# Kernel tuning notes

Hardware: AMD Instinct MI355X
Metric: run time of the kernel (lower is better)

The kernel has to match this reference:

```python
import jax, jax.numpy as jnp
import numpy as np


def setup_inputs() -> dict:
    key = jax.random.key(0)
    ks = jax.random.split(key, 7)
    d_in, d_out, batch = 4096, 4096, 8192
    x = jax.random.normal(ks[0], (batch, d_in), dtype=jnp.float32)
    w_loc = jax.random.normal(ks[1], (d_in, d_out), dtype=jnp.float32) * (1.0 / np.sqrt(d_in))
    w_std = jnp.full((d_in, d_out), -6.0, dtype=jnp.float32) + 0.1 * jax.random.normal(ks[2], (d_in, d_out), dtype=jnp.float32)
    b_loc = jax.random.normal(ks[3], (1, d_out), dtype=jnp.float32) * 0.02
    b_std = jnp.full((1, d_out), -6.0, dtype=jnp.float32) + 0.1 * jax.random.normal(ks[4], (1, d_out), dtype=jnp.float32)
    eps_w = jax.random.normal(ks[5], (d_in, d_out), dtype=jnp.float32)
    eps_b = jax.random.normal(ks[6], (1, d_out), dtype=jnp.float32)
    return {"x": x, "w_loc": w_loc, "w_std": w_std, "b_loc": b_loc, "b_std": b_std, "eps_w": eps_w, "eps_b": eps_b}


def reference(x, w_loc, w_std, b_loc, b_std, eps_w, eps_b):
    # Reparameterized sample: W ~ Normal(w_loc, softplus(w_std))
    w = w_loc + jax.nn.softplus(w_std) * eps_w          # [d_in, d_out]
    b = b_loc + jax.nn.softplus(b_std) * eps_b          # [1, d_out]
    return x @ w + b                                    # [batch, d_out]
```

## Files before the change

kernel.cpp:

```cpp
#include <hip/hip_runtime.h>

typedef unsigned short u16;
typedef unsigned int u32;
typedef __bf16 bf16;
typedef __attribute__((ext_vector_type(8))) bf16 bf16x8;
typedef __attribute__((ext_vector_type(4))) float f32x4;
typedef __attribute__((ext_vector_type(8))) u16 u16x8;

#define M_DIM 8192
#define N_DIM 4096
#define K_DIM 4096
#define NT    (K_DIM / 32)

__device__ __forceinline__ u16 f2bf(float f) {
    u32 u = __float_as_uint(f);
    u32 r = (u + 0x7fffu + ((u >> 16) & 1u)) >> 16;
    return (u16)r;
}

__device__ __forceinline__ float softplus_f(float x) {
    return fmaxf(x, 0.f) + log1pf(expf(-fabsf(x)));
}

__device__ __forceinline__ void gload_lds16(const void* g, void* l) {
    __builtin_amdgcn_global_load_lds(
        (const __attribute__((address_space(1))) void*)g,
        (__attribute__((address_space(3))) void*)l,
        16, 0, 0);
}

__global__ void conv_x_kernel(const float* __restrict__ x, u16* __restrict__ xb,
                              long long n8) {
    long long idx = blockIdx.x * (long long)blockDim.x + threadIdx.x;
    long long stride = gridDim.x * (long long)blockDim.x;
    for (long long i = idx; i < n8; i += stride) {
        const float4* xp = (const float4*)(x + i * 8);
        float4 a = xp[0], b = xp[1];
        u16x8 r;
        r[0] = f2bf(a.x); r[1] = f2bf(a.y); r[2] = f2bf(a.z); r[3] = f2bf(a.w);
        r[4] = f2bf(b.x); r[5] = f2bf(b.y); r[6] = f2bf(b.z); r[7] = f2bf(b.w);
        *(u16x8*)(xb + i * 8) = r;
    }
}

__global__ void wconv_kernel(const float* __restrict__ w_loc,
                             const float* __restrict__ w_std,
                             const float* __restrict__ eps_w,
                             u16* __restrict__ wt) {
    __shared__ u16 t[64][66];
    const int kb = blockIdx.x & 63;
    const int nb = blockIdx.x >> 6;
    const int k0 = kb * 64, n0 = nb * 64;
    const int tx = threadIdx.x & 63;
    const int ty = threadIdx.x >> 6;
#pragma unroll
    for (int r = 0; r < 64; r += 4) {
        const size_t off = (size_t)(k0 + r + ty) * N_DIM + n0 + tx;
        float v = w_loc[off] + softplus_f(w_std[off]) * eps_w[off];
        t[r + ty][tx] = f2bf(v);
    }
    __syncthreads();
#pragma unroll
    for (int r = 0; r < 64; r += 4) {
        wt[(size_t)(n0 + r + ty) * K_DIM + k0 + tx] = t[tx][r + ty];
    }
}

__global__ void bias_kernel(const float* __restrict__ b_loc,
                            const float* __restrict__ b_std,
                            const float* __restrict__ eps_b,
                            float* __restrict__ bias) {
    int i = blockIdx.x * blockDim.x + threadIdx.x;
    if (i < N_DIM) bias[i] = b_loc[i] + softplus_f(b_std[i]) * eps_b[i];
}

__global__ __launch_bounds__(512, 2) void gemm_kernel(
    const u16* __restrict__ Xb, const u16* __restrict__ Wt,
    const float* __restrict__ bias, float* __restrict__ C) {
    __shared__ __align__(16) u16 lds[32768];

    const int tid = threadIdx.x;
    const int l  = tid & 63;
    const int w  = tid >> 6;
    const int wm = w >> 2;
    const int wn = w & 3;

    const int swz = (blockIdx.x & 7) * 64 + (blockIdx.x >> 3);
    const int m0 = (swz >> 4) * 256;
    const int n0 = (swz & 15) * 256;

    const u16* Ab = Xb + (size_t)m0 * K_DIM;
    const u16* Bb = Wt + (size_t)n0 * K_DIM;

    const int sr = w * 16 + (l >> 2);
    const int sc = ((l & 3) ^ ((l >> 3) & 3)) << 3;

    const int fr = l & 15, hi = l >> 4;
    const int ce = ((hi ^ ((fr >> 1) & 3)) << 3);

    auto stageA = [&](int buf, int half, int kt) {
        const u16* g = Ab + (size_t)(half * 128 + sr) * K_DIM + kt * 32 + sc;
        gload_lds16(g, &lds[buf * 8192 + half * 4096 + w * 512]);
    };
    auto stageB = [&](int buf, int half, int kt) {
        const u16* g = Bb + (size_t)(half * 128 + sr) * K_DIM + kt * 32 + sc;
        gload_lds16(g, &lds[16384 + buf * 8192 + half * 4096 + w * 512]);
    };
    auto ldA = [&](int buf, int m) -> bf16x8 {
        return *(const bf16x8*)&lds[buf * 8192 + wm * 4096 + (m * 16 + fr) * 32 + ce];
    };
    auto ldB = [&](int buf, int n) -> bf16x8 {
        return *(const bf16x8*)&lds[16384 + buf * 8192 + (wn >> 1) * 4096
                                    + ((wn & 1) * 64 + n * 16 + fr) * 32 + ce];
    };

    f32x4 acc[8][4] = {};

    stageA(0, 0, 0); stageA(0, 1, 0); stageB(0, 0, 0); stageB(0, 1, 0);
    stageB(1, 0, 1); stageB(1, 1, 1);
    asm volatile("s_waitcnt vmcnt(2)" ::: "memory");
    __builtin_amdgcn_sched_barrier(0);
    __builtin_amdgcn_s_barrier();

    for (int t = 0; t < NT; ++t) {
        const int buf = t & 1;

        bf16x8 b[4], a[4];
        b[0] = ldB(buf, 0); b[1] = ldB(buf, 1); b[2] = ldB(buf, 2); b[3] = ldB(buf, 3);
        a[0] = ldA(buf, 0); a[1] = ldA(buf, 1); a[2] = ldA(buf, 2); a[3] = ldA(buf, 3);
        if (t + 1 < NT) { stageA(buf ^ 1, 0, t + 1); stageA(buf ^ 1, 1, t + 1); }
        __builtin_amdgcn_s_barrier();
        asm volatile("s_waitcnt lgkmcnt(0)" ::: "memory");
        __builtin_amdgcn_sched_barrier(0);
        __builtin_amdgcn_s_setprio(1);
#pragma unroll
        for (int i = 0; i < 4; ++i)
#pragma unroll
            for (int n = 0; n < 4; ++n)
                acc[i][n] = __builtin_amdgcn_mfma_f32_16x16x32_bf16(
                    a[i], b[n], acc[i][n], 0, 0, 0);
        __builtin_amdgcn_s_setprio(0);
        __builtin_amdgcn_s_barrier();

        a[0] = ldA(buf, 4); a[1] = ldA(buf, 5); a[2] = ldA(buf, 6); a[3] = ldA(buf, 7);
        if (t + 2 < NT) { stageB(buf, 0, t + 2); stageB(buf, 1, t + 2); }
        __builtin_amdgcn_s_barrier();
        asm volatile("s_waitcnt lgkmcnt(0)" ::: "memory");
        __builtin_amdgcn_sched_barrier(0);
        __builtin_amdgcn_s_setprio(1);
#pragma unroll
        for (int i = 0; i < 4; ++i)
#pragma unroll
            for (int n = 0; n < 4; ++n)
                acc[4 + i][n] = __builtin_amdgcn_mfma_f32_16x16x32_bf16(
                    a[i], b[n], acc[4 + i][n], 0, 0, 0);
        __builtin_amdgcn_s_setprio(0);
        if (t + 2 < NT) {
            asm volatile("s_waitcnt vmcnt(2)" ::: "memory");
        } else if (t + 1 < NT) {
            asm volatile("s_waitcnt vmcnt(0)" ::: "memory");
        }
        __builtin_amdgcn_sched_barrier(0);
        __builtin_amdgcn_s_barrier();
    }

    const int orow0 = m0 + wm * 128;
    const int ocol0 = n0 + wn * 64;
    float bv[4];
#pragma unroll
    for (int n = 0; n < 4; ++n) bv[n] = bias[ocol0 + n * 16 + fr];
#pragma unroll
    for (int m = 0; m < 8; ++m)
#pragma unroll
        for (int n = 0; n < 4; ++n)
#pragma unroll
            for (int j = 0; j < 4; ++j)
                C[(size_t)(orow0 + m * 16 + hi * 4 + j) * N_DIM
                  + ocol0 + n * 16 + fr] = acc[m][n][j] + bv[n];
}

extern "C" void kernel_launch(void* const* d_in, const int* in_sizes, int n_in,
                              void* d_out, int out_size, void* d_ws, size_t ws_size,
                              hipStream_t stream) {
    const float* x     = (const float*)d_in[0];
    const float* w_loc = (const float*)d_in[1];
    const float* w_std = (const float*)d_in[2];
    const float* b_loc = (const float*)d_in[3];
    const float* b_std = (const float*)d_in[4];
    const float* eps_w = (const float*)d_in[5];
    const float* eps_b = (const float*)d_in[6];
    float* out = (float*)d_out;

    char* ws = (char*)d_ws;
    u16* Xb   = (u16*)ws;
    u16* Wt   = (u16*)(ws + (size_t)M_DIM * K_DIM * 2);
    float* bv = (float*)(ws + (size_t)M_DIM * K_DIM * 2
                            + (size_t)N_DIM * K_DIM * 2);

    conv_x_kernel<<<2048, 256, 0, stream>>>(x, Xb, (long long)M_DIM * K_DIM / 8);
    wconv_kernel<<<(K_DIM / 64) * (N_DIM / 64), 256, 0, stream>>>(w_loc, w_std, eps_w, Wt);
    bias_kernel<<<N_DIM / 256, 256, 0, stream>>>(b_loc, b_std, eps_b, bv);
    gemm_kernel<<<(M_DIM / 256) * (N_DIM / 256), 512, 0, stream>>>(Xb, Wt, bv, out);
}
```

Before: 354.9 us.

## Deepen GEMM K-tile to 64 with 8-way XOR-swizzled LDS layout

Doubles the K depth of each staged tile from 32 to 64 and moves LDS to 128KB of dynamic shared memory. The LDS layout changes to 64-element rows with an 8-way XOR swizzle, and each iteration now runs four MFMA phases split across the two K halves. The aim is fewer loop iterations and vmcnt waits per K, plus longer contiguous global loads. The trade-off is that 128KB of LDS per block likely allows only one block per CU instead of the two requested by launch bounds, which reduces latency hiding.

```diff
diff --git a/kernel.cpp b/kernel.cpp
--- a/kernel.cpp
+++ b/kernel.cpp
@@ -10,7 +10,7 @@
 #define M_DIM 8192
 #define N_DIM 4096
 #define K_DIM 4096
-#define NT    (K_DIM / 32)
+#define NTK   (K_DIM / 64)
 
 __device__ __forceinline__ u16 f2bf(float f) {
     u32 u = __float_as_uint(f);
@@ -74,10 +74,26 @@
     if (i < N_DIM) bias[i] = b_loc[i] + softplus_f(b_std[i]) * eps_b[i];
 }
 
+#define MFMA_Q(O, AV, BV)                                                    \
+    _Pragma("unroll") for (int i_ = 0; i_ < 4; ++i_)                         \
+    _Pragma("unroll") for (int n_ = 0; n_ < 4; ++n_)                         \
+        acc[(O) + i_][n_] = __builtin_amdgcn_mfma_f32_16x16x32_bf16(         \
+            AV[i_], BV[n_], acc[(O) + i_][n_], 0, 0, 0);
+
+#define PH_SYNC_IN()                                                         \
+    __builtin_amdgcn_s_barrier();                                            \
+    asm volatile("s_waitcnt lgkmcnt(0)" ::: "memory");                       \
+    __builtin_amdgcn_sched_barrier(0);                                       \
+    __builtin_amdgcn_s_setprio(1);
+
+#define PH_SYNC_OUT()                                                        \
+    __builtin_amdgcn_s_setprio(0);                                           \
+    __builtin_amdgcn_s_barrier();
+
 __global__ __launch_bounds__(512, 2) void gemm_kernel(
     const u16* __restrict__ Xb, const u16* __restrict__ Wt,
     const float* __restrict__ bias, float* __restrict__ C) {
-    __shared__ __align__(16) u16 lds[32768];
+    extern __shared__ u16 lds[];
 
     const int tid = threadIdx.x;
     const int l  = tid & 63;
@@ -92,72 +108,82 @@
     const u16* Ab = Xb + (size_t)m0 * K_DIM;
     const u16* Bb = Wt + (size_t)n0 * K_DIM;
 
-    const int sr = w * 16 + (l >> 2);
-    const int sc = ((l & 3) ^ ((l >> 3) & 3)) << 3;
+    const int srow = tid >> 3;
+    const int sq   = ((tid & 7) ^ (srow & 7)) * 8;
 
     const int fr = l & 15, hi = l >> 4;
-    const int ce = ((hi ^ ((fr >> 1) & 3)) << 3);
-
-    auto stageA = [&](int buf, int half, int kt) {
-        const u16* g = Ab + (size_t)(half * 128 + sr) * K_DIM + kt * 32 + sc;
-        gload_lds16(g, &lds[buf * 8192 + half * 4096 + w * 512]);
+    const int cg0 = (hi ^ (fr & 7)) * 8;
+    const int cg1 = cg0 ^ 32;
+
+    auto stageA = [&](int u) {
+#pragma unroll
+        for (int s = 0; s < 4; ++s) {
+            const u16* g = Ab + (size_t)(s * 64 + srow) * K_DIM + u * 64 + sq;
+            gload_lds16(g, &lds[(u & 1) * 16384 + s * 4096 + tid * 8]);
+        }
     };
-    auto stageB = [&](int buf, int half, int kt) {
-        const u16* g = Bb + (size_t)(half * 128 + sr) * K_DIM + kt * 32 + sc;
-        gload_lds16(g, &lds[16384 + buf * 8192 + half * 4096 + w * 512]);
+    auto stageB = [&](int u) {
+#pragma unroll
+        for (int s = 0; s < 4; ++s) {
+            const u16* g = Bb + (size_t)(s * 64 + srow) * K_DIM + u * 64 + sq;
+            gload_lds16(g, &lds[32768 + (u & 1) * 16384 + s * 4096 + tid * 8]);
+        }
     };
-    auto ldA = [&](int buf, int m) -> bf16x8 {
-        return *(const bf16x8*)&lds[buf * 8192 + wm * 4096 + (m * 16 + fr) * 32 + ce];
-    };
-    auto ldB = [&](int buf, int n) -> bf16x8 {
-        return *(const bf16x8*)&lds[16384 + buf * 8192 + (wn >> 1) * 4096
-                                    + ((wn & 1) * 64 + n * 16 + fr) * 32 + ce];
-    };
 
     f32x4 acc[8][4] = {};
 
-    stageA(0, 0, 0); stageA(0, 1, 0); stageB(0, 0, 0); stageB(0, 1, 0);
-    stageB(1, 0, 1); stageB(1, 1, 1);
-    asm volatile("s_waitcnt vmcnt(2)" ::: "memory");
+    stageA(0); stageB(0); stageB(1);
+    asm volatile("s_waitcnt vmcnt(4)" ::: "memory");
     __builtin_amdgcn_sched_barrier(0);
     __builtin_amdgcn_s_barrier();
 
-    for (int t = 0; t < NT; ++t) {
-        const int buf = t & 1;
-
-        bf16x8 b[4], a[4];
-        b[0] = ldB(buf, 0); b[1] = ldB(buf, 1); b[2] = ldB(buf, 2); b[3] = ldB(buf, 3);
-        a[0] = ldA(buf, 0); a[1] = ldA(buf, 1); a[2] = ldA(buf, 2); a[3] = ldA(buf, 3);
-        if (t + 1 < NT) { stageA(buf ^ 1, 0, t + 1); stageA(buf ^ 1, 1, t + 1); }
+    for (int u = 0; u < NTK; ++u) {
+        const int bo = (u & 1) * 16384;
+        const int bB = 32768 + bo;
+        const int arow = bo + (wm * 128 + fr) * 64;
+        const int brow = bB + (wn * 64 + fr) * 64;
+        bf16x8 a[4], b0[4], b1[4];
+
+#pragma unroll
+        for (int n = 0; n < 4; ++n) {
+            b0[n] = *(const bf16x8*)&lds[brow + n * 1024 + cg0];
+            b1[n] = *(const bf16x8*)&lds[brow + n * 1024 + cg1];
+        }
+#pragma unroll
+        for (int m = 0; m < 4; ++m)
+            a[m] = *(const bf16x8*)&lds[arow + m * 1024 + cg0];
+        if (u + 1 < NTK) stageA(u + 1);
+        PH_SYNC_IN();
+        MFMA_Q(0, a, b0);
+        PH_SYNC_OUT();
+
+#pragma unroll
+        for (int m = 0; m < 4; ++m)
+            a[m] = *(const bf16x8*)&lds[arow + (m + 4) * 1024 + cg0];
+        if (u + 2 < NTK) stageB(u + 2);
+        PH_SYNC_IN();
+        MFMA_Q(4, a, b0);
+        PH_SYNC_OUT();
+
+#pragma unroll
+        for (int m = 0; m < 4; ++m)
+            a[m] = *(const bf16x8*)&lds[arow + m * 1024 + cg1];
+        PH_SYNC_IN();
+        MFMA_Q(0, a, b1);
+        PH_SYNC_OUT();
+
+#pragma unroll
+        for (int m = 0; m < 4; ++m)
+            a[m] = *(const bf16x8*)&lds[arow + (m + 4) * 1024 + cg1];
         __builtin_amdgcn_s_barrier();
         asm volatile("s_waitcnt lgkmcnt(0)" ::: "memory");
         __builtin_amdgcn_sched_barrier(0);
         __builtin_amdgcn_s_setprio(1);
-#pragma unroll
-        for (int i = 0; i < 4; ++i)
-#pragma unroll
-            for (int n = 0; n < 4; ++n)
-                acc[i][n] = __builtin_amdgcn_mfma_f32_16x16x32_bf16(
-                    a[i], b[n], acc[i][n], 0, 0, 0);
+        MFMA_Q(4, a, b1);
         __builtin_amdgcn_s_setprio(0);
-        __builtin_amdgcn_s_barrier();
-
-        a[0] = ldA(buf, 4); a[1] = ldA(buf, 5); a[2] = ldA(buf, 6); a[3] = ldA(buf, 7);
-        if (t + 2 < NT) { stageB(buf, 0, t + 2); stageB(buf, 1, t + 2); }
-        __builtin_amdgcn_s_barrier();
-        asm volatile("s_waitcnt lgkmcnt(0)" ::: "memory");
-        __builtin_amdgcn_sched_barrier(0);
-        __builtin_amdgcn_s_setprio(1);
-#pragma unroll
-        for (int i = 0; i < 4; ++i)
-#pragma unroll
-            for (int n = 0; n < 4; ++n)
-                acc[4 + i][n] = __builtin_amdgcn_mfma_f32_16x16x32_bf16(
-                    a[i], b[n], acc[4 + i][n], 0, 0, 0);
-        __builtin_amdgcn_s_setprio(0);
-        if (t + 2 < NT) {
-            asm volatile("s_waitcnt vmcnt(2)" ::: "memory");
-        } else if (t + 1 < NT) {
+        if (u + 2 < NTK) {
+            asm volatile("s_waitcnt vmcnt(4)" ::: "memory");
+        } else if (u + 1 < NTK) {
             asm volatile("s_waitcnt vmcnt(0)" ::: "memory");
         }
         __builtin_amdgcn_sched_barrier(0);
@@ -197,8 +223,11 @@
     float* bv = (float*)(ws + (size_t)M_DIM * K_DIM * 2
                             + (size_t)N_DIM * K_DIM * 2);
 
+    (void)hipFuncSetAttribute((const void*)gemm_kernel,
+                              hipFuncAttributeMaxDynamicSharedMemorySize, 131072);
+
     conv_x_kernel<<<2048, 256, 0, stream>>>(x, Xb, (long long)M_DIM * K_DIM / 8);
     wconv_kernel<<<(K_DIM / 64) * (N_DIM / 64), 256, 0, stream>>>(w_loc, w_std, eps_w, Wt);
     bias_kernel<<<N_DIM / 256, 256, 0, stream>>>(b_loc, b_std, eps_b, bv);
-    gemm_kernel<<<(M_DIM / 256) * (N_DIM / 256), 512, 0, stream>>>(Xb, Wt, bv, out);
-}
+    gemm_kernel<<<(M_DIM / 256) * (N_DIM / 256), 512, 131072, stream>>>(Xb, Wt, bv, out);
+}
```

After: 354.6 us. About the same (-0.1%).

## Deepen GEMM K-tile to 64 with triple-buffered B in dynamic LDS

Applied to the files above, without the earlier changes.

The GEMM main loop now processes 64-wide K tiles with a 128-byte-row XOR swizzle. A is double-buffered and B is triple-buffered in 160KB of dynamic shared memory. Each half-step issues 32 MFMAs per wave with a single barrier per iteration, cutting synchronisation and LDS-load overhead per unit of K. The larger LDS footprint likely limits residency to one block per CU, reducing latency hiding from co-resident blocks.

```diff
diff --git a/kernel.cpp b/kernel.cpp
--- a/kernel.cpp
+++ b/kernel.cpp
@@ -10,7 +10,7 @@
 #define M_DIM 8192
 #define N_DIM 4096
 #define K_DIM 4096
-#define NT    (K_DIM / 32)
+#define NTK   (K_DIM / 64)
 
 __device__ __forceinline__ u16 f2bf(float f) {
     u32 u = __float_as_uint(f);
@@ -77,7 +77,7 @@
 __global__ __launch_bounds__(512, 2) void gemm_kernel(
     const u16* __restrict__ Xb, const u16* __restrict__ Wt,
     const float* __restrict__ bias, float* __restrict__ C) {
-    __shared__ __align__(16) u16 lds[32768];
+    extern __shared__ __align__(16) u16 lds[];
 
     const int tid = threadIdx.x;
     const int l  = tid & 63;
@@ -92,91 +92,100 @@
     const u16* Ab = Xb + (size_t)m0 * K_DIM;
     const u16* Bb = Wt + (size_t)n0 * K_DIM;
 
-    const int sr = w * 16 + (l >> 2);
-    const int sc = ((l & 3) ^ ((l >> 3) & 3)) << 3;
+    const int srow = tid >> 3;
+    const int sq   = ((tid & 7) ^ (srow & 7)) * 8;
 
     const int fr = l & 15, hi = l >> 4;
-    const int ce = ((hi ^ ((fr >> 1) & 3)) << 3);
-
-    auto stageA = [&](int buf, int half, int kt) {
-        const u16* g = Ab + (size_t)(half * 128 + sr) * K_DIM + kt * 32 + sc;
-        gload_lds16(g, &lds[buf * 8192 + half * 4096 + w * 512]);
+    const int g0 = (hi ^ (fr & 7)) << 3;
+
+    auto stageA = [&](int u, int h) {
+#pragma unroll
+        for (int s = 0; s < 2; ++s) {
+            const u16* g = Ab + (size_t)(h * 128 + s * 64 + srow) * K_DIM + u * 64 + sq;
+            gload_lds16(g, &lds[(u & 1) * 16384 + h * 8192 + s * 4096 + tid * 8]);
+        }
     };
-    auto stageB = [&](int buf, int half, int kt) {
-        const u16* g = Bb + (size_t)(half * 128 + sr) * K_DIM + kt * 32 + sc;
-        gload_lds16(g, &lds[16384 + buf * 8192 + half * 4096 + w * 512]);
+    auto stageB = [&](int u, int slot, int h) {
+#pragma unroll
+        for (int s = 0; s < 2; ++s) {
+            const u16* g = Bb + (size_t)(h * 128 + s * 64 + srow) * K_DIM + u * 64 + sq;
+            gload_lds16(g, &lds[32768 + slot * 16384 + h * 8192 + s * 4096 + tid * 8]);
+        }
     };
-    auto ldA = [&](int buf, int m) -> bf16x8 {
-        return *(const bf16x8*)&lds[buf * 8192 + wm * 4096 + (m * 16 + fr) * 32 + ce];
-    };
-    auto ldB = [&](int buf, int n) -> bf16x8 {
-        return *(const bf16x8*)&lds[16384 + buf * 8192 + (wn >> 1) * 4096
-                                    + ((wn & 1) * 64 + n * 16 + fr) * 32 + ce];
-    };
 
     f32x4 acc[8][4] = {};
 
-    stageA(0, 0, 0); stageA(0, 1, 0); stageB(0, 0, 0); stageB(0, 1, 0);
-    stageB(1, 0, 1); stageB(1, 1, 1);
-    asm volatile("s_waitcnt vmcnt(2)" ::: "memory");
+    stageA(0, 0); stageA(0, 1);
+    stageB(0, 0, 0); stageB(0, 0, 1);
+    stageB(1, 1, 0); stageB(1, 1, 1);
+    asm volatile("s_waitcnt vmcnt(4)" ::: "memory");
     __builtin_amdgcn_sched_barrier(0);
     __builtin_amdgcn_s_barrier();
 
-    for (int t = 0; t < NT; ++t) {
-        const int buf = t & 1;
-
-        bf16x8 b[4], a[4];
-        b[0] = ldB(buf, 0); b[1] = ldB(buf, 1); b[2] = ldB(buf, 2); b[3] = ldB(buf, 3);
-        a[0] = ldA(buf, 0); a[1] = ldA(buf, 1); a[2] = ldA(buf, 2); a[3] = ldA(buf, 3);
-        if (t + 1 < NT) { stageA(buf ^ 1, 0, t + 1); stageA(buf ^ 1, 1, t + 1); }
-        __builtin_amdgcn_s_barrier();
+#define MFMA32()                                                              \
+    _Pragma("unroll") for (int mb = 0; mb < 8; ++mb)                          \
+    _Pragma("unroll") for (int nb = 0; nb < 4; ++nb)                          \
+        acc[mb][nb] = __builtin_amdgcn_mfma_f32_16x16x32_bf16(                \
+            a[mb], b[nb], acc[mb][nb], 0, 0, 0);
+
+    int scur = 0, snxt = 2;
+    for (int u = 0; u < NTK; ++u) {
+        const int ab = (u & 1) * 16384 + (wm * 128 + fr) * 64;
+        const int bb = 32768 + scur * 16384 + (wn * 64 + fr) * 64;
+        bf16x8 a[8], b[4];
+
+#pragma unroll
+        for (int nb = 0; nb < 4; ++nb)
+            b[nb] = *(const bf16x8*)&lds[bb + nb * 1024 + g0];
+#pragma unroll
+        for (int mb = 0; mb < 8; ++mb)
+            a[mb] = *(const bf16x8*)&lds[ab + mb * 1024 + g0];
+        if (u + 1 < NTK) { stageA(u + 1, 0); stageA(u + 1, 1); }
         asm volatile("s_waitcnt lgkmcnt(0)" ::: "memory");
         __builtin_amdgcn_sched_barrier(0);
         __builtin_amdgcn_s_setprio(1);
-#pragma unroll
-        for (int i = 0; i < 4; ++i)
-#pragma unroll
-            for (int n = 0; n < 4; ++n)
-                acc[i][n] = __builtin_amdgcn_mfma_f32_16x16x32_bf16(
-                    a[i], b[n], acc[i][n], 0, 0, 0);
+        MFMA32();
         __builtin_amdgcn_s_setprio(0);
-        __builtin_amdgcn_s_barrier();
-
-        a[0] = ldA(buf, 4); a[1] = ldA(buf, 5); a[2] = ldA(buf, 6); a[3] = ldA(buf, 7);
-        if (t + 2 < NT) { stageB(buf, 0, t + 2); stageB(buf, 1, t + 2); }
-        __builtin_amdgcn_s_barrier();
+
+#pragma unroll
+        for (int nb = 0; nb < 4; ++nb)
+            b[nb] = *(const bf16x8*)&lds[bb + nb * 1024 + (g0 ^ 32)];
+#pragma unroll
+        for (int mb = 0; mb < 8; ++mb)
+            a[mb] = *(const bf16x8*)&lds[ab + mb * 1024 + (g0 ^ 32)];
+        if (u + 2 < NTK) { stageB(u + 2, snxt, 0); stageB(u + 2, snxt, 1); }
         asm volatile("s_waitcnt lgkmcnt(0)" ::: "memory");
         __builtin_amdgcn_sched_barrier(0);
         __builtin_amdgcn_s_setprio(1);
-#pragma unroll
-        for (int i = 0; i < 4; ++i)
-#pragma unroll
-            for (int n = 0; n < 4; ++n)
-                acc[4 + i][n] = __builtin_amdgcn_mfma_f32_16x16x32_bf16(
-                    a[i], b[n], acc[4 + i][n], 0, 0, 0);
+        MFMA32();
         __builtin_amdgcn_s_setprio(0);
-        if (t + 2 < NT) {
-            asm volatile("s_waitcnt vmcnt(2)" ::: "memory");
-        } else if (t + 1 < NT) {
+
+        if (u + 2 < NTK) {
+            asm volatile("s_waitcnt vmcnt(4)" ::: "memory");
+        } else if (u + 1 < NTK) {
             asm volatile("s_waitcnt vmcnt(0)" ::: "memory");
         }
         __builtin_amdgcn_sched_barrier(0);
         __builtin_amdgcn_s_barrier();
-    }
+
+        scur = (scur == 2) ? 0 : scur + 1;
+        snxt = (snxt == 2) ? 0 : snxt + 1;
+    }
+#undef MFMA32
 
     const int orow0 = m0 + wm * 128;
     const int ocol0 = n0 + wn * 64;
     float bv[4];
 #pragma unroll
-    for (int n = 0; n < 4; ++n) bv[n] = bias[ocol0 + n * 16 + fr];
-#pragma unroll
-    for (int m = 0; m < 8; ++m)
-#pragma unroll
-        for (int n = 0; n < 4; ++n)
+    for (int nb = 0; nb < 4; ++nb) bv[nb] = bias[ocol0 + nb * 16 + fr];
+#pragma unroll
+    for (int mb = 0; mb < 8; ++mb)
+#pragma unroll
+        for (int nb = 0; nb < 4; ++nb)
 #pragma unroll
             for (int j = 0; j < 4; ++j)
-                C[(size_t)(orow0 + m * 16 + hi * 4 + j) * N_DIM
-                  + ocol0 + n * 16 + fr] = acc[m][n][j] + bv[n];
+                C[(size_t)(orow0 + mb * 16 + hi * 4 + j) * N_DIM
+                  + ocol0 + nb * 16 + fr] = acc[mb][nb][j] + bv[nb];
 }
 
 extern "C" void kernel_launch(void* const* d_in, const int* in_sizes, int n_in,
@@ -197,8 +206,11 @@
     float* bv = (float*)(ws + (size_t)M_DIM * K_DIM * 2
                             + (size_t)N_DIM * K_DIM * 2);
 
+    (void)hipFuncSetAttribute((const void*)gemm_kernel,
+                              hipFuncAttributeMaxDynamicSharedMemorySize, 163840);
+
     conv_x_kernel<<<2048, 256, 0, stream>>>(x, Xb, (long long)M_DIM * K_DIM / 8);
     wconv_kernel<<<(K_DIM / 64) * (N_DIM / 64), 256, 0, stream>>>(w_loc, w_std, eps_w, Wt);
     bias_kernel<<<N_DIM / 256, 256, 0, stream>>>(b_loc, b_std, eps_b, bv);
-    gemm_kernel<<<(M_DIM / 256) * (N_DIM / 256), 512, 0, stream>>>(Xb, Wt, bv, out);
-}
+    gemm_kernel<<<(M_DIM / 256) * (N_DIM / 256), 512, 163840, stream>>>(Xb, Wt, bv, out);
+}
```

Result: faster. 326.2 us (-8.1%).
